# Optimization experiments

Measured on AMD Instinct MI355X. Metric: run time of the kernel, lower is better.

Reference implementation:

```python
import jax, jax.numpy as jnp
import numpy as np

D = 512      # model dim
NH = 8       # heads
DH = 64      # dim per head
M = 256      # num landmarks
ITERS = 6    # pinv iterations
EPS = 1e-5   # layernorm eps


def layer_norm(x, g, b):
    mu = x.mean(-1, keepdims=True)
    var = ((x - mu) ** 2).mean(-1, keepdims=True)
    return (x - mu) * jax.lax.rsqrt(var + EPS) * g + b


def moore_penrose_pinv(x, iters=ITERS):
    abs_x = jnp.abs(x)
    col = abs_x.sum(-1)
    row = abs_x.sum(-2)
    z = jnp.swapaxes(x, -1, -2) / (jnp.max(col) * jnp.max(row))
    I = jnp.eye(x.shape[-1], dtype=x.dtype)
    for _ in range(iters):
        xz = x @ z
        z = 0.25 * z @ (13 * I - xz @ (15 * I - xz @ (7 * I - xz)))
    return z


def nystrom_attention(x, w_qkv, w_out, b_out, res_w):
    B, n0, _ = x.shape
    pad = (M - n0 % M) % M
    x = jnp.pad(x, ((0, 0), (pad, 0), (0, 0)))  # pad at front, like lucidrains
    n = n0 + pad
    qkv = x @ w_qkv  # (B, n, 3*D), no bias
    q, k, v = jnp.split(qkv, 3, axis=-1)
    rs = lambda t: t.reshape(B, n, NH, DH).transpose(0, 2, 1, 3)  # (B,H,n,d)
    q = rs(q) * (DH ** -0.5)
    k = rs(k)
    v = rs(v)
    l = n // M
    q_l = q.reshape(B, NH, M, l, DH).mean(3)  # (B,H,M,d) landmark means
    k_l = k.reshape(B, NH, M, l, DH).mean(3)
    s1 = jnp.einsum('bhnd,bhmd->bhnm', q, k_l)
    s2 = jnp.einsum('bhmd,bhld->bhml', q_l, k_l)
    s3 = jnp.einsum('bhmd,bhnd->bhmn', q_l, k)
    a1 = jax.nn.softmax(s1, -1)
    a2 = jax.nn.softmax(s2, -1)
    a3 = jax.nn.softmax(s3, -1)
    out = a1 @ (moore_penrose_pinv(a2) @ (a3 @ v))  # (B,H,n,d)
    # depthwise residual conv over sequence: Conv2d(heads, heads, (33,1), groups=heads)
    res = jax.lax.conv_general_dilated(v, res_w, (1, 1), 'SAME',
                                       feature_group_count=NH,
                                       dimension_numbers=('NCHW', 'OIHW', 'NCHW'))
    out = out + res
    out = out.transpose(0, 2, 1, 3).reshape(B, n, NH * DH) @ w_out + b_out
    return out[:, -n0:]


def dwconv(x, w, b):
    y = jax.lax.conv_general_dilated(x, w, (1, 1), 'SAME',
                                     feature_group_count=x.shape[1],
                                     dimension_numbers=('NCHW', 'OIHW', 'NCHW'))
    return y + b[None, :, None, None]


def ppeg(x, pw7, pb7, pw5, pb5, pw3, pb3, Hh, Ww):
    cls, feat = x[:, :1], x[:, 1:]
    B, _, C = x.shape
    cnn = feat.transpose(0, 2, 1).reshape(B, C, Hh, Ww)
    y = cnn + dwconv(cnn, pw7, pb7) + dwconv(cnn, pw5, pb5) + dwconv(cnn, pw3, pb3)
    y = y.reshape(B, C, Hh * Ww).transpose(0, 2, 1)
    return jnp.concatenate([cls, y], axis=1)


def _forward(x, w_fc1, b_fc1, cls_token, ln1_g, ln1_b, qkv1_w, out1_w, out1_b, res1_w,
             ln2_g, ln2_b, qkv2_w, out2_w, out2_b, res2_w,
             pw7, pb7, pw5, pb5, pw3, pb3, lnf_g, lnf_b, w_fc2, b_fc2):
    h = jax.nn.relu(x @ w_fc1 + b_fc1)  # (B, N, 512)
    Hn = h.shape[1]
    s = int(np.ceil(np.sqrt(Hn)))  # static grid side
    add = s * s - Hn
    h = jnp.concatenate([h, h[:, :add]], axis=1)
    B = h.shape[0]
    cls = jnp.broadcast_to(cls_token, (B, 1, D))
    h = jnp.concatenate([cls, h], axis=1)
    h = h + nystrom_attention(layer_norm(h, ln1_g, ln1_b), qkv1_w, out1_w, out1_b, res1_w)
    h = ppeg(h, pw7, pb7, pw5, pb5, pw3, pb3, s, s)
    h = h + nystrom_attention(layer_norm(h, ln2_g, ln2_b), qkv2_w, out2_w, out2_b, res2_w)
    h = layer_norm(h, lnf_g, lnf_b)[:, 0]
    return h @ w_fc2 + b_fc2


def setup_inputs() -> dict:
    key = jax.random.key(0)
    ks = jax.random.split(key, 16)
    g = lambda k, shp, s=0.02: jax.random.normal(k, shp, dtype=jnp.float32) * s
    z = lambda n: jnp.zeros((n,), jnp.float32)
    o = lambda n: jnp.ones((n,), jnp.float32)
    B, N, DIN, NC = 2, 10000, 1024, 2
    return {
        'x': jax.random.normal(ks[0], (B, N, DIN), dtype=jnp.float32),
        'w_fc1': g(ks[1], (DIN, D)), 'b_fc1': z(D),
        'cls_token': g(ks[2], (1, 1, D), 1.0),
        'ln1_g': o(D), 'ln1_b': z(D),
        'qkv1_w': g(ks[3], (D, 3 * D)),
        'out1_w': g(ks[4], (D, D)), 'out1_b': z(D),
        'res1_w': g(ks[5], (NH, 1, 33, 1)),
        'ln2_g': o(D), 'ln2_b': z(D),
        'qkv2_w': g(ks[6], (D, 3 * D)),
        'out2_w': g(ks[7], (D, D)), 'out2_b': z(D),
        'res2_w': g(ks[8], (NH, 1, 33, 1)),
        'pw7': g(ks[9], (D, 1, 7, 7)), 'pb7': z(D),
        'pw5': g(ks[10], (D, 1, 5, 5)), 'pb5': z(D),
        'pw3': g(ks[11], (D, 1, 3, 3)), 'pb3': z(D),
        'lnf_g': o(D), 'lnf_b': z(D),
        'w_fc2': g(ks[12], (D, NC)), 'b_fc2': z(NC),
    }


def reference(x, w_fc1, b_fc1, cls_token, ln1_g, ln1_b, qkv1_w, out1_w, out1_b, res1_w,
              ln2_g, ln2_b, qkv2_w, out2_w, out2_b, res2_w,
              pw7, pb7, pw5, pb5, pw3, pb3, lnf_g, lnf_b, w_fc2, b_fc2):
    logits = _forward(x, w_fc1, b_fc1, cls_token, ln1_g, ln1_b, qkv1_w, out1_w, out1_b, res1_w,
                      ln2_g, ln2_b, qkv2_w, out2_w, out2_b, res2_w,
                      pw7, pb7, pw5, pb5, pw3, pb3, lnf_g, lnf_b, w_fc2, b_fc2)
    Y_prob = jax.nn.softmax(logits, -1)
    Y_hat = jnp.argmax(logits, -1)
    return logits, Y_prob, Y_hat
```

## Files before the change

kernel.cpp:

```cpp
#include <hip/hip_runtime.h>
#include <math.h>

#define FLAG_RELU 1
#define FLAG_BIAS 2
#define FLAG_ACC  4
#define FLAG_ATOMIC 8

static constexpr int BB   = 2;
static constexpr int N0   = 10000;
static constexpr int DIN  = 1024;
static constexpr int D    = 512;
static constexpr int NH   = 8;
static constexpr int DH   = 64;
static constexpr int MM   = 256;
static constexpr int SEQ  = 10240;
static constexpr int PADR = 239;
static constexpr int NTOK = 10001;
static constexpr int LL   = 40;
static constexpr float EPS_ = 1e-5f;

typedef short short8v __attribute__((ext_vector_type(8)));
typedef float f32x4 __attribute__((ext_vector_type(4)));

__device__ __forceinline__ void atomicMaxPosF(float* addr, float v) {
    atomicMax((unsigned int*)addr, __float_as_uint(v));
}
__device__ __forceinline__ ushort f2bf(float f) {
    unsigned u = __float_as_uint(f);
    return (ushort)((u + 0x7FFFu + ((u >> 16) & 1u)) >> 16);
}
__device__ __forceinline__ float bf2f(ushort h) {
    return __uint_as_float(((unsigned)h) << 16);
}
__device__ __forceinline__ void split4(float4 f, ushort* ph, ushort* pl) {
    ushort4 hv, lv;
    hv.x = f2bf(f.x); lv.x = f2bf(f.x - bf2f(hv.x));
    hv.y = f2bf(f.y); lv.y = f2bf(f.y - bf2f(hv.y));
    hv.z = f2bf(f.z); lv.z = f2bf(f.z - bf2f(hv.z));
    hv.w = f2bf(f.w); lv.w = f2bf(f.w - bf2f(hv.w));
    *(ushort4*)ph = hv; *(ushort4*)pl = lv;
}

__global__ __launch_bounds__(256)
void mgemm128(const float* __restrict__ A, int lda, long long sAz,
              const ushort* __restrict__ BtH, const ushort* __restrict__ BtL, int ldbt,
              float* __restrict__ C, int ldc, long long sCz, const float* __restrict__ bias,
              int M, int N, int K, int flags, int qcols, float qscale)
{
    __shared__ ushort AsH[4*128*8], AsL[4*128*8], BsH[4*128*8], BsL[4*128*8];
    A += (size_t)blockIdx.z * sAz;
    C += (size_t)blockIdx.z * sCz;
    int t = threadIdx.x;
    int m0 = blockIdx.y * 128, n0 = blockIdx.x * 128;
    int w = t >> 6, lane = t & 63, q = lane >> 4, r = lane & 15;
    int wm = w >> 1, wn = w & 1;
    f32x4 acc[4][4];
    #pragma unroll
    for (int i = 0; i < 4; i++)
        #pragma unroll
        for (int j = 0; j < 4; j++) acc[i][j] = (f32x4){0.f,0.f,0.f,0.f};

    int srow = t >> 1, scg = (t & 1) * 16;
    int qg = (t & 1) * 2;
    int gm = m0 + srow;
    float4 pa0, pa1, pa2, pa3;
    uint4  pb0, pb1, pb2, pb3;
    {
        pa0 = pa1 = pa2 = pa3 = make_float4(0,0,0,0);
        if (gm < M) {
            const float* ap = A + (size_t)gm * lda + scg;
            pa0 = *(const float4*)(ap);   pa1 = *(const float4*)(ap+4);
            pa2 = *(const float4*)(ap+8); pa3 = *(const float4*)(ap+12);
        }
        size_t gb = (size_t)(n0 + srow) * ldbt + scg;
        pb0 = *(const uint4*)(BtH + gb); pb1 = *(const uint4*)(BtH + gb + 8);
        pb2 = *(const uint4*)(BtL + gb); pb3 = *(const uint4*)(BtL + gb + 8);
    }
    for (int k0 = 0; k0 < K; k0 += 32) {
        {
            ushort hb[16], lb[16];
            split4(pa0, &hb[0],  &lb[0]);
            split4(pa1, &hb[4],  &lb[4]);
            split4(pa2, &hb[8],  &lb[8]);
            split4(pa3, &hb[12], &lb[12]);
            *(uint4*)&AsH[(qg  )*1024 + srow*8] = *(uint4*)&hb[0];
            *(uint4*)&AsH[(qg+1)*1024 + srow*8] = *(uint4*)&hb[8];
            *(uint4*)&AsL[(qg  )*1024 + srow*8] = *(uint4*)&lb[0];
            *(uint4*)&AsL[(qg+1)*1024 + srow*8] = *(uint4*)&lb[8];
            *(uint4*)&BsH[(qg  )*1024 + srow*8] = pb0;
            *(uint4*)&BsH[(qg+1)*1024 + srow*8] = pb1;
            *(uint4*)&BsL[(qg  )*1024 + srow*8] = pb2;
            *(uint4*)&BsL[(qg+1)*1024 + srow*8] = pb3;
        }
        __syncthreads();
        if (k0 + 32 < K) {
            pa0 = pa1 = pa2 = pa3 = make_float4(0,0,0,0);
            if (gm < M) {
                const float* ap = A + (size_t)gm * lda + k0 + 32 + scg;
                pa0 = *(const float4*)(ap);   pa1 = *(const float4*)(ap+4);
                pa2 = *(const float4*)(ap+8); pa3 = *(const float4*)(ap+12);
            }
            size_t gb = (size_t)(n0 + srow) * ldbt + k0 + 32 + scg;
            pb0 = *(const uint4*)(BtH + gb); pb1 = *(const uint4*)(BtH + gb + 8);
            pb2 = *(const uint4*)(BtL + gb); pb3 = *(const uint4*)(BtL + gb + 8);
        }
        short8v ah[4], al[4];
        #pragma unroll
        for (int mi = 0; mi < 4; mi++) {
            int row = wm*64 + mi*16 + r;
            ah[mi] = *(const short8v*)&AsH[q*1024 + row*8];
            al[mi] = *(const short8v*)&AsL[q*1024 + row*8];
        }
        #pragma unroll
        for (int ni = 0; ni < 4; ni++) {
            int col = wn*64 + ni*16 + r;
            short8v bh = *(const short8v*)&BsH[q*1024 + col*8];
            short8v bl = *(const short8v*)&BsL[q*1024 + col*8];
            #pragma unroll
            for (int mi = 0; mi < 4; mi++) {
                acc[mi][ni] = __builtin_amdgcn_mfma_f32_16x16x32_bf16(ah[mi], bh, acc[mi][ni], 0,0,0);
                acc[mi][ni] = __builtin_amdgcn_mfma_f32_16x16x32_bf16(ah[mi], bl, acc[mi][ni], 0,0,0);
                acc[mi][ni] = __builtin_amdgcn_mfma_f32_16x16x32_bf16(al[mi], bh, acc[mi][ni], 0,0,0);
            }
        }
        __syncthreads();
    }
    #pragma unroll
    for (int mi = 0; mi < 4; mi++)
        #pragma unroll
        for (int ni = 0; ni < 4; ni++) {
            int gcol = n0 + wn*64 + ni*16 + r;
            float qs = (gcol < qcols) ? qscale : 1.f;
            float bv = (flags & FLAG_BIAS) ? bias[gcol] : 0.f;
            #pragma unroll
            for (int rg = 0; rg < 4; rg++) {
                int grow = m0 + wm*64 + mi*16 + q*4 + rg;
                if (grow >= M) continue;
                float v = acc[mi][ni][rg] * qs + bv;
                if (flags & FLAG_RELU) v = fmaxf(v, 0.f);
                float* cp = C + (size_t)grow * ldc + gcol;
                if (flags & FLAG_ACC) v += *cp;
                *cp = v;
            }
        }
}

__global__ __launch_bounds__(256)
void mbgemm64(const float* __restrict__ Abase, long long sAb, long long sAh, long long sAz, int lda,
              const ushort* __restrict__ BtH, const ushort* __restrict__ BtL,
              const float* __restrict__ Bnt, long long sBb, long long sBh, int ldb,
              float* __restrict__ Cbase, long long sCb, long long sCh, long long sCz, int ldc,
              ushort* __restrict__ eTH, ushort* __restrict__ eTL, long long sT, int ldct,
              int M, int N, int K, int nchunk,
              float dg, float bsc, float osc, int slab0, int flags)
{
    __shared__ ushort AsH[4*64*8], AsL[4*64*8], BsH[4*64*8], BsL[4*64*8];
    int zi = blockIdx.z / nchunk, ch = blockIdx.z % nchunk;
    int g = slab0 + zi, b = g >> 3, h = g & 7;
    const float* A = Abase + (size_t)b*sAb + (size_t)h*sAh + (size_t)zi*sAz;
    float* C = Cbase ? (Cbase + (size_t)b*sCb + (size_t)h*sCh + (size_t)zi*sCz) : nullptr;
    int kpc = K / nchunk;
    int kb = ch * kpc, ke = kb + kpc;
    int t = threadIdx.x;
    int m0 = blockIdx.y * 64, n0 = blockIdx.x * 64;
    int w = t >> 6, lane = t & 63, q = lane >> 4, r = lane & 15;
    int wm = w >> 1, wn = w & 1;
    f32x4 acc[2][2];
    #pragma unroll
    for (int i = 0; i < 2; i++)
        #pragma unroll
        for (int j = 0; j < 2; j++) acc[i][j] = (f32x4){0.f,0.f,0.f,0.f};

    int srow = t >> 2, scg = (t & 3) * 8;
    int qg = t & 3;
    const float* Abp = Bnt ? (Bnt + (size_t)b*sBb + (size_t)h*sBh) : nullptr;
    float4 pa0, pa1;
    float4 pf0, pf1;
    uint4  pu0, pu1;
    {
        const float* ap = A + (size_t)(m0 + srow) * lda + kb + scg;
        pa0 = *(const float4*)ap; pa1 = *(const float4*)(ap+4);
        if (Bnt) {
            const float* bp = Abp + (size_t)(n0 + srow) * ldb + kb + scg;
            pf0 = *(const float4*)bp; pf1 = *(const float4*)(bp+4);
        } else {
            size_t gb = (size_t)b*sBb + (size_t)h*sBh + (size_t)(n0 + srow) * ldb + kb + scg;
            pu0 = *(const uint4*)(BtH + gb); pu1 = *(const uint4*)(BtL + gb);
        }
    }
    for (int k0 = kb; k0 < ke; k0 += 32) {
        {
            ushort hb[8], lb[8];
            split4(pa0, &hb[0], &lb[0]);
            split4(pa1, &hb[4], &lb[4]);
            *(uint4*)&AsH[qg*512 + srow*8] = *(uint4*)&hb[0];
            *(uint4*)&AsL[qg*512 + srow*8] = *(uint4*)&lb[0];
            if (Bnt) {
                ushort hc[8], lc[8];
                split4(pf0, &hc[0], &lc[0]);
                split4(pf1, &hc[4], &lc[4]);
                *(uint4*)&BsH[qg*512 + srow*8] = *(uint4*)&hc[0];
                *(uint4*)&BsL[qg*512 + srow*8] = *(uint4*)&lc[0];
            } else {
                *(uint4*)&BsH[qg*512 + srow*8] = pu0;
                *(uint4*)&BsL[qg*512 + srow*8] = pu1;
            }
        }
        __syncthreads();
        if (k0 + 32 < ke) {
            const float* ap = A + (size_t)(m0 + srow) * lda + k0 + 32 + scg;
            pa0 = *(const float4*)ap; pa1 = *(const float4*)(ap+4);
            if (Bnt) {
                const float* bp = Abp + (size_t)(n0 + srow) * ldb + k0 + 32 + scg;
                pf0 = *(const float4*)bp; pf1 = *(const float4*)(bp+4);
            } else {
                size_t gb = (size_t)b*sBb + (size_t)h*sBh + (size_t)(n0 + srow) * ldb + k0 + 32 + scg;
                pu0 = *(const uint4*)(BtH + gb); pu1 = *(const uint4*)(BtL + gb);
            }
        }
        short8v ah[2], al[2];
        #pragma unroll
        for (int mi = 0; mi < 2; mi++) {
            int row = wm*32 + mi*16 + r;
            ah[mi] = *(const short8v*)&AsH[q*512 + row*8];
            al[mi] = *(const short8v*)&AsL[q*512 + row*8];
        }
        #pragma unroll
        for (int ni = 0; ni < 2; ni++) {
            int col = wn*32 + ni*16 + r;
            short8v bh = *(const short8v*)&BsH[q*512 + col*8];
            short8v bl = *(const short8v*)&BsL[q*512 + col*8];
            #pragma unroll
            for (int mi = 0; mi < 2; mi++) {
                acc[mi][ni] = __builtin_amdgcn_mfma_f32_16x16x32_bf16(ah[mi], bh, acc[mi][ni], 0,0,0);
                acc[mi][ni] = __builtin_amdgcn_mfma_f32_16x16x32_bf16(ah[mi], bl, acc[mi][ni], 0,0,0);
                acc[mi][ni] = __builtin_amdgcn_mfma_f32_16x16x32_bf16(al[mi], bh, acc[mi][ni], 0,0,0);
            }
        }
        __syncthreads();
    }
    bool dgnz = (dg != 0.f);
    #pragma unroll
    for (int mi = 0; mi < 2; mi++)
        #pragma unroll
        for (int ni = 0; ni < 2; ni++) {
            int gm0 = m0 + wm*32 + mi*16 + q*4;
            int gn  = n0 + wn*32 + ni*16 + r;
            float v[4];
            #pragma unroll
            for (int rg = 0; rg < 4; rg++) {
                float u = bsc * acc[mi][ni][rg];
                if (dgnz) u += dg * A[(size_t)(gm0+rg) * lda + gn];
                v[rg] = osc * u;
            }
            if (C) {
                if (flags & FLAG_ATOMIC) {
                    #pragma unroll
                    for (int rg = 0; rg < 4; rg++)
                        atomicAdd(C + (size_t)(gm0+rg) * ldc + gn, v[rg]);
                } else {
                    #pragma unroll
                    for (int rg = 0; rg < 4; rg++)
                        C[(size_t)(gm0+rg) * ldc + gn] = v[rg];
                }
            }
            if (eTH) {
                ushort4 hv, lv;
                hv.x = f2bf(v[0]); lv.x = f2bf(v[0] - bf2f(hv.x));
                hv.y = f2bf(v[1]); lv.y = f2bf(v[1] - bf2f(hv.y));
                hv.z = f2bf(v[2]); lv.z = f2bf(v[2] - bf2f(hv.z));
                hv.w = f2bf(v[3]); lv.w = f2bf(v[3] - bf2f(hv.w));
                size_t to = (size_t)g * sT + (size_t)gn * ldct + gm0;
                *(ushort4*)(eTH + to) = hv;
                *(ushort4*)(eTL + to) = lv;
            }
        }
}

__global__ __launch_bounds__(256)
void convsplitT(const float* __restrict__ in, ushort* __restrict__ oh, ushort* __restrict__ ol,
                int R, int C, int ldin, long long sInB, long long sInH, long long sInZ,
                int ldo, long long sOutZ)
{
    __shared__ float tile[32][33];
    int z = blockIdx.z, b = z >> 3, h = z & 7;
    const float* I = in + (size_t)b*sInB + (size_t)h*sInH + (size_t)z*sInZ;
    int p0 = blockIdx.x * 32, c0 = blockIdx.y * 32;
    int tx = threadIdx.x & 31, ty = threadIdx.x >> 5;
    #pragma unroll
    for (int k = 0; k < 4; k++) {
        int rr = p0 + ty + k*8, cc = c0 + tx;
        tile[ty + k*8][tx] = (rr < R && cc < C) ? I[(size_t)rr * ldin + cc] : 0.f;
    }
    __syncthreads();
    #pragma unroll
    for (int k = 0; k < 4; k++) {
        int rr = p0 + tx, cc = c0 + ty + k*8;
        if (rr < R && cc < C) {
            float f = tile[tx][ty + k*8];
            ushort hv = f2bf(f);
            size_t o = (size_t)z * sOutZ + (size_t)cc * ldo + rr;
            oh[o] = hv; ol[o] = f2bf(f - bf2f(hv));
        }
    }
}

__global__ void fill_cls(const float* __restrict__ cls, float* __restrict__ H) {
    H[(size_t)blockIdx.x * NTOK * D + threadIdx.x] = cls[threadIdx.x];
}

__global__ __launch_bounds__(256)
void ln_pad(const float* __restrict__ H, const float* __restrict__ g,
            const float* __restrict__ bt, float* __restrict__ out)
{
    int blk = blockIdx.x;
    int b = blk / SEQ, i = blk % SEQ;
    int t = threadIdx.x;
    float* orow = out + (size_t)blk * D;
    if (i < PADR) { orow[t] = 0.f; orow[t+256] = 0.f; return; }
    const float* x = H + ((size_t)b * NTOK + (i - PADR)) * D;
    float v0 = x[t], v1 = x[t+256];
    __shared__ float w1[4], w2[4];
    float s = v0 + v1;
    for (int o = 32; o > 0; o >>= 1) s += __shfl_xor(s, o);
    if ((t & 63) == 0) w1[t >> 6] = s;
    __syncthreads();
    float mu = (w1[0]+w1[1]+w1[2]+w1[3]) * (1.0f / D);
    float d0 = v0 - mu, d1 = v1 - mu;
    float qq = d0*d0 + d1*d1;
    for (int o = 32; o > 0; o >>= 1) qq += __shfl_xor(qq, o);
    if ((t & 63) == 0) w2[t >> 6] = qq;
    __syncthreads();
    float rs = rsqrtf((w2[0]+w2[1]+w2[2]+w2[3]) * (1.0f / D) + EPS_);
    orow[t]     = d0 * rs * g[t]     + bt[t];
    orow[t+256] = d1 * rs * g[t+256] + bt[t+256];
}

__global__ __launch_bounds__(512)
void landmarks(const float* __restrict__ qkv, float* __restrict__ ql,
               float* __restrict__ klt, ushort* __restrict__ klH, ushort* __restrict__ klL)
{
    int blk = blockIdx.x;
    int b = blk >> 8, m = blk & 255;
    int c = threadIdx.x;
    const float* base = qkv + ((size_t)b * SEQ + (size_t)m * LL) * 1536;
    float sq0=0,sq1=0,sq2=0,sq3=0, sk0=0,sk1=0,sk2=0,sk3=0;
    for (int tt = 0; tt < LL; tt += 4) {
        const float* rr = base + (size_t)tt * 1536;
        sq0 += rr[c];          sk0 += rr[512 + c];
        sq1 += rr[1536 + c];   sk1 += rr[1536 + 512 + c];
        sq2 += rr[3072 + c];   sk2 += rr[3072 + 512 + c];
        sq3 += rr[4608 + c];   sk3 += rr[4608 + 512 + c];
    }
    float sq = (sq0+sq1+sq2+sq3) * (1.0f / LL);
    float sk = (sk0+sk1+sk2+sk3) * (1.0f / LL);
    int h = c >> 6, d = c & 63;
    int slab = b * NH + h;
    ql [((size_t)slab * MM + m) * DH + d] = sq;
    klt[((size_t)slab * DH + d) * MM + m] = sk;
    size_t kidx = ((size_t)slab * MM + m) * DH + d;
    ushort kh = f2bf(sk);
    klH[kidx] = kh; klL[kidx] = f2bf(sk - bf2f(kh));
}

__global__ __launch_bounds__(256)
void s2_softmax(const float* __restrict__ ql, const float* __restrict__ klt,
                float* __restrict__ a2)
{
    int blk = blockIdx.x;
    int m = blk & 255, slab = blk >> 8;
    int j = threadIdx.x;
    __shared__ float q[64];
    __shared__ float red[256];
    if (j < 64) q[j] = ql[((size_t)slab * MM + m) * DH + j];
    __syncthreads();
    const float* kt = klt + (size_t)slab * DH * MM;
    float s = 0.f;
    #pragma unroll 8
    for (int kk = 0; kk < 64; kk++) s = fmaf(q[kk], kt[kk*MM + j], s);
    red[j] = s; __syncthreads();
    for (int o = 128; o > 0; o >>= 1) { if (j < o) red[j] = fmaxf(red[j], red[j+o]); __syncthreads(); }
    float mx = red[0]; __syncthreads();
    float e = expf(s - mx);
    red[j] = e; __syncthreads();
    for (int o = 128; o > 0; o >>= 1) { if (j < o) red[j] += red[j+o]; __syncthreads(); }
    a2[((size_t)slab * MM + m) * MM + j] = e / red[0];
}

__global__ void zero_scr(float* s) { if (threadIdx.x < 2) s[threadIdx.x] = 0.f; }

__global__ __launch_bounds__(256)
void a2_alpha(const float* __restrict__ a2, float* __restrict__ scr)
{
    int slab = blockIdx.x, t = threadIdx.x;
    const float* A = a2 + (size_t)slab * MM * MM;
    float cs = 0.f, rs = 0.f;
    for (int rr = 0; rr < MM; rr++) cs += fabsf(A[(size_t)rr * MM + t]);
    for (int cc = 0; cc < MM; cc++) rs += fabsf(A[(size_t)t * MM + cc]);
    __shared__ float red[256];
    red[t] = rs; __syncthreads();
    for (int o = 128; o > 0; o >>= 1) { if (t < o) red[t] = fmaxf(red[t], red[t+o]); __syncthreads(); }
    float mrs = red[0]; __syncthreads();
    red[t] = cs; __syncthreads();
    for (int o = 128; o > 0; o >>= 1) { if (t < o) red[t] = fmaxf(red[t], red[t+o]); __syncthreads(); }
    float mcs = red[0];
    if (t == 0) { atomicMaxPosF(scr + 0, mrs); atomicMaxPosF(scr + 1, mcs); }
}

__global__ __launch_bounds__(256)
void z_init(const float* __restrict__ a2, const float* __restrict__ scr,
            float* __restrict__ z, ushort* __restrict__ zTh, ushort* __restrict__ zTl)
{
    size_t idx = (size_t)blockIdx.x * 256 + threadIdx.x;
    int slab = (int)(idx >> 16), rr = (int)((idx >> 8) & 255), cc = (int)(idx & 255);
    float inv = 1.0f / (scr[0] * scr[1]);
    z[idx] = a2[((size_t)slab << 16) + (size_t)cc * MM + rr] * inv;
    float tv = a2[idx] * inv;
    ushort th = f2bf(tv);
    zTh[idx] = th; zTl[idx] = f2bf(tv - bf2f(th));
}

__global__ __launch_bounds__(256)
void s3_softmax(float* __restrict__ s3)
{
    float* row = s3 + (size_t)blockIdx.x * SEQ;
    int t = threadIdx.x;
    float4 v[10];
    #pragma unroll
    for (int i = 0; i < 10; i++) v[i] = *(const float4*)(row + 4*(i*256 + t));
    float mx = -3.4e38f;
    #pragma unroll
    for (int i = 0; i < 10; i++)
        mx = fmaxf(mx, fmaxf(fmaxf(v[i].x, v[i].y), fmaxf(v[i].z, v[i].w)));
    __shared__ float red[4];
    for (int o = 32; o > 0; o >>= 1) mx = fmaxf(mx, __shfl_xor(mx, o));
    if ((t & 63) == 0) red[t >> 6] = mx;
    __syncthreads();
    mx = fmaxf(fmaxf(red[0], red[1]), fmaxf(red[2], red[3]));
    float sum = 0.f;
    #pragma unroll
    for (int i = 0; i < 10; i++) {
        v[i].x = expf(v[i].x - mx); v[i].y = expf(v[i].y - mx);
        v[i].z = expf(v[i].z - mx); v[i].w = expf(v[i].w - mx);
        sum += v[i].x + v[i].y + v[i].z + v[i].w;
    }
    __shared__ float red2[4];
    for (int o = 32; o > 0; o >>= 1) sum += __shfl_xor(sum, o);
    if ((t & 63) == 0) red2[t >> 6] = sum;
    __syncthreads();
    float inv = 1.0f / (red2[0] + red2[1] + red2[2] + red2[3]);
    #pragma unroll
    for (int i = 0; i < 10; i++) {
        v[i].x *= inv; v[i].y *= inv; v[i].z *= inv; v[i].w *= inv;
        *(float4*)(row + 4*(i*256 + t)) = v[i];
    }
}

__global__ __launch_bounds__(256)
void softmax256(float* __restrict__ P)
{
    int wid = threadIdx.x >> 6, lane = threadIdx.x & 63;
    float* p = P + ((size_t)blockIdx.x * 4 + wid) * MM + lane * 4;
    float4 v = *(float4*)p;
    float m = fmaxf(fmaxf(v.x, v.y), fmaxf(v.z, v.w));
    for (int o = 32; o > 0; o >>= 1) m = fmaxf(m, __shfl_xor(m, o));
    v.x = expf(v.x - m); v.y = expf(v.y - m);
    v.z = expf(v.z - m); v.w = expf(v.w - m);
    float s = v.x + v.y + v.z + v.w;
    for (int o = 32; o > 0; o >>= 1) s += __shfl_xor(s, o);
    float inv = 1.0f / s;
    v.x *= inv; v.y *= inv; v.z *= inv; v.w *= inv;
    *(float4*)p = v;
}

__global__ __launch_bounds__(512)
void res_add(const float* __restrict__ qkv, const float* __restrict__ rw,
             float* __restrict__ attn)
{
    int blk = blockIdx.x;
    int b = blk / (SEQ/16), i0 = (blk % (SEQ/16)) * 16;
    int c = threadIdx.x, h = c >> 6;
    __shared__ float w[NH*33];
    if (c < NH*33) w[c] = rw[c];
    __syncthreads();
    float acc[16];
    float* ab = attn + ((size_t)b * SEQ + i0) * D + c;
    #pragma unroll
    for (int rr = 0; rr < 16; rr++) acc[rr] = ab[(size_t)rr * D];
    const float* vb = qkv + (size_t)b * SEQ * 1536 + 2*D + c;
    const float* wh = w + h * 33;
    #pragma unroll 4
    for (int jj = 0; jj < 48; jj++) {
        int j = i0 + jj - 16;
        float val = ((unsigned)j < (unsigned)SEQ) ? vb[(size_t)j * 1536] : 0.f;
        #pragma unroll
        for (int rr = 0; rr < 16; rr++) {
            int ky = jj - rr;
            if (ky >= 0 && ky < 33) acc[rr] = fmaf(val, wh[ky], acc[rr]);
        }
    }
    #pragma unroll
    for (int rr = 0; rr < 16; rr++) ab[(size_t)rr * D] = acc[rr];
}

__global__ __launch_bounds__(256)
void t_fw(const float* __restrict__ H, float* __restrict__ P)
{
    __shared__ float tile[32][33];
    int p0 = blockIdx.x * 32, c0 = blockIdx.y * 32, b = blockIdx.z;
    int tx = threadIdx.x & 31, ty = threadIdx.x >> 5;
    #pragma unroll
    for (int k = 0; k < 4; k++) {
        int pos = p0 + ty + k*8;
        tile[ty + k*8][tx] = (pos < 10000)
            ? H[((size_t)b * NTOK + 1 + pos) * D + c0 + tx] : 0.f;
    }
    __syncthreads();
    #pragma unroll
    for (int k = 0; k < 4; k++) {
        int c = c0 + ty + k*8, pos = p0 + tx;
        if (pos < 10000)
            P[((size_t)b * D + c) * 10000 + pos] = tile[tx][ty + k*8];
    }
}

__global__ __launch_bounds__(256)
void ppeg_conv(const float* __restrict__ P,
               const float* __restrict__ w7, const float* __restrict__ b7,
               const float* __restrict__ w5, const float* __restrict__ b5,
               const float* __restrict__ w3, const float* __restrict__ b3,
               float* __restrict__ Q)
{
    __shared__ float PS[106 * 107];
    __shared__ float w7s[49], w5s[25], w3s[9];
    int blk = blockIdx.x;
    int b = blk >> 9, c = blk & 511;
    int t = threadIdx.x;
    for (int idx = t; idx < 106*107; idx += 256) PS[idx] = 0.f;
    if (t < 49) w7s[t] = w7[(size_t)c * 49 + t];
    if (t < 25) w5s[t] = w5[(size_t)c * 25 + t];
    if (t < 9)  w3s[t] = w3[(size_t)c * 9 + t];
    float bsum = b7[c] + b5[c] + b3[c];
    __syncthreads();
    const float* Pin = P + ((size_t)b * D + c) * 10000;
    for (int p = t; p < 10000; p += 256) {
        int y = p / 100, x = p - y * 100;
        PS[(y + 3) * 107 + x + 3] = Pin[p];
    }
    __syncthreads();
    float* Qo = Q + ((size_t)b * D + c) * 10000;
    for (int task = t; task < 2500; task += 256) {
        int ry = task / 100, x = task - ry * 100;
        int y0 = ry * 4;
        float a0 = bsum + PS[(y0+3)*107 + x+3];
        float a1 = bsum + PS[(y0+4)*107 + x+3];
        float a2 = bsum + PS[(y0+5)*107 + x+3];
        float a3 = bsum + PS[(y0+6)*107 + x+3];
        #pragma unroll
        for (int rr = 0; rr < 10; rr++) {
            const float* rp = &PS[(y0 + rr) * 107 + x];
            #pragma unroll
            for (int kx = 0; kx < 7; kx++) {
                float v = rp[kx];
                if (rr < 7)            a0 = fmaf(v, w7s[rr*7 + kx], a0);
                if (rr >= 1 && rr < 8) a1 = fmaf(v, w7s[(rr-1)*7 + kx], a1);
                if (rr >= 2 && rr < 9) a2 = fmaf(v, w7s[(rr-2)*7 + kx], a2);
                if (rr >= 3)           a3 = fmaf(v, w7s[(rr-3)*7 + kx], a3);
            }
        }
        #pragma unroll
        for (int rr = 0; rr < 8; rr++) {
            const float* rp = &PS[(y0 + rr + 1) * 107 + x + 1];
            #pragma unroll
            for (int kx = 0; kx < 5; kx++) {
                float v = rp[kx];
                if (rr < 5)            a0 = fmaf(v, w5s[rr*5 + kx], a0);
                if (rr >= 1 && rr < 6) a1 = fmaf(v, w5s[(rr-1)*5 + kx], a1);
                if (rr >= 2 && rr < 7) a2 = fmaf(v, w5s[(rr-2)*5 + kx], a2);
                if (rr >= 3)           a3 = fmaf(v, w5s[(rr-3)*5 + kx], a3);
            }
        }
        #pragma unroll
        for (int rr = 0; rr < 6; rr++) {
            const float* rp = &PS[(y0 + rr + 2) * 107 + x + 2];
            #pragma unroll
            for (int kx = 0; kx < 3; kx++) {
                float v = rp[kx];
                if (rr < 3)            a0 = fmaf(v, w3s[rr*3 + kx], a0);
                if (rr >= 1 && rr < 4) a1 = fmaf(v, w3s[(rr-1)*3 + kx], a1);
                if (rr >= 2 && rr < 5) a2 = fmaf(v, w3s[(rr-2)*3 + kx], a2);
                if (rr >= 3)           a3 = fmaf(v, w3s[(rr-3)*3 + kx], a3);
            }
        }
        Qo[(y0+0)*100 + x] = a0;
        Qo[(y0+1)*100 + x] = a1;
        Qo[(y0+2)*100 + x] = a2;
        Qo[(y0+3)*100 + x] = a3;
    }
}

__global__ __launch_bounds__(256)
void t_bw(const float* __restrict__ Q, float* __restrict__ H)
{
    __shared__ float tile[32][33];
    int p0 = blockIdx.x * 32, c0 = blockIdx.y * 32, b = blockIdx.z;
    int tx = threadIdx.x & 31, ty = threadIdx.x >> 5;
    #pragma unroll
    for (int k = 0; k < 4; k++) {
        int c = c0 + ty + k*8, pos = p0 + tx;
        tile[ty + k*8][tx] = (pos < 10000)
            ? Q[((size_t)b * D + c) * 10000 + pos] : 0.f;
    }
    __syncthreads();
    #pragma unroll
    for (int k = 0; k < 4; k++) {
        int pos = p0 + ty + k*8;
        if (pos < 10000)
            H[((size_t)b * NTOK + 1 + pos) * D + c0 + tx] = tile[tx][ty + k*8];
    }
}

__global__ __launch_bounds__(512)
void final_head(const float* __restrict__ H, const float* __restrict__ g,
                const float* __restrict__ bt, const float* __restrict__ w2,
                const float* __restrict__ b2, float* __restrict__ out)
{
    int b = blockIdx.x, t = threadIdx.x;
    __shared__ float red[512];
    float v = H[(size_t)b * NTOK * D + t];
    red[t] = v; __syncthreads();
    for (int o = 256; o > 0; o >>= 1) { if (t < o) red[t] += red[t+o]; __syncthreads(); }
    float mu = red[0] * (1.0f / D); __syncthreads();
    float dv = v - mu;
    red[t] = dv*dv; __syncthreads();
    for (int o = 256; o > 0; o >>= 1) { if (t < o) red[t] += red[t+o]; __syncthreads(); }
    float rstd = rsqrtf(red[0] * (1.0f / D) + EPS_); __syncthreads();
    float xn = dv * rstd * g[t] + bt[t];
    red[t] = xn * w2[2*t]; __syncthreads();
    for (int o = 256; o > 0; o >>= 1) { if (t < o) red[t] += red[t+o]; __syncthreads(); }
    float l0 = red[0] + b2[0]; __syncthreads();
    red[t] = xn * w2[2*t+1]; __syncthreads();
    for (int o = 256; o > 0; o >>= 1) { if (t < o) red[t] += red[t+o]; __syncthreads(); }
    float l1 = red[0] + b2[1];
    if (t == 0) {
        out[b*2+0] = l0; out[b*2+1] = l1;
        float mx = fmaxf(l0, l1);
        float e0 = expf(l0 - mx), e1 = expf(l1 - mx);
        float ssum = e0 + e1;
        out[4 + b*2 + 0] = e0 / ssum;
        out[4 + b*2 + 1] = e1 / ssum;
        out[8 + b] = (l1 > l0) ? 1.0f : 0.0f;
    }
}

extern "C" void kernel_launch(void* const* d_in, const int* in_sizes, int n_in,
                              void* d_out, int out_size, void* d_ws, size_t ws_size,
                              hipStream_t stream)
{
    const float* x      = (const float*)d_in[0];
    const float* w_fc1  = (const float*)d_in[1];
    const float* b_fc1  = (const float*)d_in[2];
    const float* cls    = (const float*)d_in[3];
    const float* ln1_g  = (const float*)d_in[4];
    const float* ln1_b  = (const float*)d_in[5];
    const float* qkv1_w = (const float*)d_in[6];
    const float* out1_w = (const float*)d_in[7];
    const float* out1_b = (const float*)d_in[8];
    const float* res1_w = (const float*)d_in[9];
    const float* ln2_g  = (const float*)d_in[10];
    const float* ln2_b  = (const float*)d_in[11];
    const float* qkv2_w = (const float*)d_in[12];
    const float* out2_w = (const float*)d_in[13];
    const float* out2_b = (const float*)d_in[14];
    const float* res2_w = (const float*)d_in[15];
    const float* pw7 = (const float*)d_in[16];
    const float* pb7 = (const float*)d_in[17];
    const float* pw5 = (const float*)d_in[18];
    const float* pb5 = (const float*)d_in[19];
    const float* pw3 = (const float*)d_in[20];
    const float* pb3 = (const float*)d_in[21];
    const float* lnf_g = (const float*)d_in[22];
    const float* lnf_b = (const float*)d_in[23];
    const float* w_fc2 = (const float*)d_in[24];
    const float* b_fc2 = (const float*)d_in[25];

    float* ws = (float*)d_ws;
    size_t off = 0;
    auto alloc = [&](size_t n) { float* p = ws + off; off += (n + 63) & ~(size_t)63; return p; };
    float* H    = alloc((size_t)BB * NTOK * D);
    float* LN   = alloc((size_t)BB * SEQ * D);
    float* QKV  = alloc((size_t)BB * SEQ * 3 * D);
    float* QL   = alloc((size_t)BB * NH * MM * DH);
    float* KLT  = alloc((size_t)BB * NH * DH * MM);
    float* A2   = alloc((size_t)BB * NH * MM * MM);
    float* ZA   = alloc((size_t)BB * NH * MM * MM);
    float* ZB   = alloc((size_t)BB * NH * MM * MM);
    float* XZ   = alloc((size_t)BB * NH * MM * MM);
    float* A3V  = alloc((size_t)BB * NH * MM * DH);
    float* WB   = alloc((size_t)BB * NH * MM * DH);
    float* S3   = alloc((size_t)8 * MM * SEQ);
    float* SCR  = alloc(64);
    auto ualloc = [&](size_t n) { ushort* p = (ushort*)(ws + off); off += ((n + 127) / 2) & ~(size_t)63; return p; };
    ushort* WTfcH = ualloc((size_t)512 * 1024);
    ushort* WTfcL = ualloc((size_t)512 * 1024);
    ushort* WTqH  = ualloc((size_t)1536 * 512);
    ushort* WTqL  = ualloc((size_t)1536 * 512);
    ushort* WToH  = ualloc((size_t)512 * 512);
    ushort* WToL  = ualloc((size_t)512 * 512);
    ushort* klBH  = ualloc((size_t)16 * MM * DH);
    ushort* klBL  = ualloc((size_t)16 * MM * DH);
    float*  ATTN = LN;
    ushort* VTH  = (ushort*)LN;
    ushort* VTL  = VTH + (size_t)16 * DH * SEQ;
    ushort* A3VTH = (ushort*)ZB;
    ushort* A3VTL = A3VTH + (size_t)16 * DH * MM;
    ushort* WBTH  = A3VTL + (size_t)16 * DH * MM;
    ushort* WBTL  = WBTH  + (size_t)16 * DH * MM;
    ushort* PT   = (ushort*)S3;
    const size_t PS_ = (size_t)16 * 65536;
    ushort* zTAH = PT;            ushort* zTAL = PT + PS_;
    ushort* zTBH = PT + 2*PS_;    ushort* zTBL = PT + 3*PS_;
    ushort* XZTH = PT + 4*PS_;    ushort* XZTL = PT + 5*PS_;
    ushort* T1TH = PT + 6*PS_;    ushort* T1TL = PT + 7*PS_;
    ushort* T2TH = PT + 8*PS_;    ushort* T2TL = PT + 9*PS_;
    (void)ws_size; (void)in_sizes; (void)n_in; (void)out_size;

    convsplitT<<<dim3(32,16,1), 256, 0, stream>>>(w_fc1, WTfcH, WTfcL, 1024, 512, 512, 0,0,0, 1024, 0);
    mgemm128<<<dim3(4, 79, BB), 256, 0, stream>>>(x, DIN, (long long)N0*DIN,
        WTfcH, WTfcL, 1024, H + D, D, (long long)NTOK*D, b_fc1,
        N0, D, DIN, FLAG_BIAS|FLAG_RELU, 0, 1.f);
    fill_cls<<<BB, D, 0, stream>>>(cls, H);

    auto attention = [&](const float* lg, const float* lb,
                         const float* qw, const float* ow,
                         const float* ob, const float* rw)
    {
        convsplitT<<<dim3(16,48,1), 256, 0, stream>>>(qw, WTqH, WTqL, 512, 1536, 1536, 0,0,0, 512, 0);
        convsplitT<<<dim3(16,16,1), 256, 0, stream>>>(ow, WToH, WToL, 512, 512, 512, 0,0,0, 512, 0);
        ln_pad<<<BB*SEQ, 256, 0, stream>>>(H, lg, lb, LN);
        mgemm128<<<dim3(12, 160, 1), 256, 0, stream>>>(LN, D, 0, WTqH, WTqL, D,
            QKV, 3*D, 0, nullptr, BB*SEQ, 3*D, D, 0, D, 0.125f);
        convsplitT<<<dim3(320, 2, 16), 256, 0, stream>>>(QKV + 2*D, VTH, VTL,
            SEQ, DH, 1536, (long long)SEQ*1536, 64, 0, SEQ, (long long)DH*SEQ);
        landmarks<<<BB*MM, 512, 0, stream>>>(QKV, QL, KLT, klBH, klBL);
        s2_softmax<<<BB*NH*MM, 256, 0, stream>>>(QL, KLT, A2);
        zero_scr<<<1, 64, 0, stream>>>(SCR);
        a2_alpha<<<BB*NH, 256, 0, stream>>>(A2, SCR);
        z_init<<<BB*NH*MM*MM/256, 256, 0, stream>>>(A2, SCR, ZA, zTAH, zTAL);
        float* z = ZA; float* zn = ZB;
        ushort *zTcH = zTAH, *zTcL = zTAL, *zTnH = zTBH, *zTnL = zTBL;
        for (int it = 0; it < 6; it++) {
            dim3 g(4, 4, 16);
            mbgemm64<<<g,256,0,stream>>>(A2, 0,0,65536LL, MM,
                zTcH, zTcL, nullptr, 8LL*65536, 65536LL, MM,
                XZ, 0,0,65536LL, MM, XZTH, XZTL, 65536LL, MM,
                MM, MM, MM, 1, 0.f, 1.f, 1.f, 0, 0);
            mbgemm64<<<g,256,0,stream>>>(XZ, 0,0,65536LL, MM,
                XZTH, XZTL, nullptr, 8LL*65536, 65536LL, MM,
                nullptr, 0,0,0, MM, T1TH, T1TL, 65536LL, MM,
                MM, MM, MM, 1, 7.f, -1.f, 1.f, 0, 0);
            mbgemm64<<<g,256,0,stream>>>(XZ, 0,0,65536LL, MM,
                T1TH, T1TL, nullptr, 8LL*65536, 65536LL, MM,
                nullptr, 0,0,0, MM, T2TH, T2TL, 65536LL, MM,
                MM, MM, MM, 1, 15.f, -1.f, 1.f, 0, 0);
            mbgemm64<<<g,256,0,stream>>>(z, 0,0,65536LL, MM,
                T2TH, T2TL, nullptr, 8LL*65536, 65536LL, MM,
                zn, 0,0,65536LL, MM, zTnH, zTnL, 65536LL, MM,
                MM, MM, MM, 1, 13.f, -1.f, 0.25f, 0, 0);
            float* ts = z; z = zn; zn = ts;
            ushort* uh = zTcH; zTcH = zTnH; zTnH = uh;
            ushort* ul = zTcL; zTcL = zTnL; zTnL = ul;
        }
        for (int grp = 0; grp < 2; grp++) {
            int slab0 = grp * 8;
            mbgemm64<<<dim3(160, 4, 8), 256, 0, stream>>>(QL, 8LL*16384, 16384LL, 0, DH,
                nullptr, nullptr, QKV + D, (long long)SEQ*1536, 64LL, 1536,
                S3, 0,0,(long long)MM*SEQ, SEQ, nullptr, nullptr, 0, 0,
                MM, SEQ, DH, 1, 0.f, 1.f, 1.f, slab0, 0);
            s3_softmax<<<8*MM, 256, 0, stream>>>(S3);
            hipMemsetAsync(A3V + (size_t)slab0 * MM * DH, 0,
                           (size_t)8 * MM * DH * sizeof(float), stream);
            mbgemm64<<<dim3(1, 4, 8*16), 256, 0, stream>>>(S3, 0,0,(long long)MM*SEQ, SEQ,
                VTH, VTL, nullptr, 8LL*DH*SEQ, (long long)DH*SEQ, SEQ,
                A3V, 8LL*16384, 16384LL, 0, DH, nullptr, nullptr, 0, 0,
                MM, DH, SEQ, 16, 0.f, 1.f, 1.f, slab0, FLAG_ATOMIC);
        }
        convsplitT<<<dim3(8, 2, 16), 256, 0, stream>>>(A3V, A3VTH, A3VTL,
            MM, DH, DH, 0, 0, 16384LL, MM, 16384LL);
        mbgemm64<<<dim3(1, 4, 16), 256, 0, stream>>>(z, 0,0,65536LL, MM,
            A3VTH, A3VTL, nullptr, 8LL*16384, 16384LL, MM,
            WB, 8LL*16384, 16384LL, 0, DH, WBTH, WBTL, 16384LL, MM,
            MM, DH, MM, 1, 0.f, 1.f, 1.f, 0, 0);
        for (int grp = 0; grp < 2; grp++) {
            int slab0 = grp * 8;
            mbgemm64<<<dim3(4, 160, 8), 256, 0, stream>>>(QKV, (long long)SEQ*1536, 64LL, 0, 1536,
                klBH, klBL, nullptr, 8LL*16384, 16384LL, DH,
                S3, 0,0,(long long)SEQ*MM, MM, nullptr, nullptr, 0, 0,
                SEQ, MM, DH, 1, 0.f, 1.f, 1.f, slab0, 0);
            softmax256<<<8*SEQ/4, 256, 0, stream>>>(S3);
            mbgemm64<<<dim3(1, 160, 8), 256, 0, stream>>>(S3, 0,0,(long long)SEQ*MM, MM,
                WBTH, WBTL, nullptr, 8LL*16384, 16384LL, MM,
                ATTN, (long long)SEQ*D, 64LL, 0, D, nullptr, nullptr, 0, 0,
                SEQ, DH, MM, 1, 0.f, 1.f, 1.f, slab0, 0);
        }
        res_add<<<BB*SEQ/16, 512, 0, stream>>>(QKV, rw, ATTN);
        mgemm128<<<dim3(4, 79, BB), 256, 0, stream>>>(ATTN + (size_t)PADR*D, D, (long long)SEQ*D,
            WToH, WToL, D, H, D, (long long)NTOK*D, ob,
            NTOK, D, D, FLAG_BIAS|FLAG_ACC, 0, 1.f);
    };

    attention(ln1_g, ln1_b, qkv1_w, out1_w, out1_b, res1_w);

    {
        float* Pp = S3;
        float* Qp = S3 + (size_t)BB * D * 10000;
        dim3 tg((10000 + 31)/32, D/32, BB);
        t_fw<<<tg, 256, 0, stream>>>(H, Pp);
        ppeg_conv<<<BB*D, 256, 0, stream>>>(Pp, pw7, pb7, pw5, pb5, pw3, pb3, Qp);
        t_bw<<<tg, 256, 0, stream>>>(Qp, H);
    }

    attention(ln2_g, ln2_b, qkv2_w, out2_w, out2_b, res2_w);

    final_head<<<BB, 512, 0, stream>>>(H, lnf_g, lnf_b, w_fc2, b_fc2, (float*)d_out);
}
```

Before: 2.390 ms.

## Fuse q·k_landmark scores, softmax, and a1@W product into one kernel

Replaces the two-group sequence of S1 GEMM, row softmax and the GEMM with the pinv-weighted matrix with a single a1_fused kernel. Each block computes a 64-token by 256-landmark score tile with split-bf16 MFMA, does the softmax in registers and shared memory, stages unnormalized probabilities in LDS, and multiplies by WB^T before normalizing. This removes the large S1 round-trips through global memory and several launches. In exchange the kernel uses about 68KB of LDS, which limits occupancy, and re-splits P from LDS using uncoalesced strided reads.

Measured after the change: 2.372 ms. Within noise of the previous version (-0.7%).

```diff
diff --git a/kernel.cpp b/kernel.cpp
--- a/kernel.cpp
+++ b/kernel.cpp
@@ -39,6 +39,12 @@
     hv.z = f2bf(f.z); lv.z = f2bf(f.z - bf2f(hv.z));
     hv.w = f2bf(f.w); lv.w = f2bf(f.w - bf2f(hv.w));
     *(ushort4*)ph = hv; *(ushort4*)pl = lv;
+}
+__device__ __forceinline__ void split8r(const float* p, short8v& h, short8v& l) {
+    ushort hb[8], lb[8];
+    split4(*(const float4*)p,     &hb[0], &lb[0]);
+    split4(*(const float4*)(p+4), &hb[4], &lb[4]);
+    h = *(short8v*)hb; l = *(short8v*)lb;
 }
 
 __global__ __launch_bounds__(256)
@@ -278,6 +284,125 @@
 }
 
 __global__ __launch_bounds__(256)
+void a1_fused(const float* __restrict__ qkv,
+              const ushort* __restrict__ klH, const ushort* __restrict__ klL,
+              const ushort* __restrict__ wbH, const ushort* __restrict__ wbL,
+              float* __restrict__ attn)
+{
+    __shared__ float Pc[256*66];
+    __shared__ float redm[4][64];
+    __shared__ float reds[4][64];
+    int g = blockIdx.y, b = g >> 3, h = g & 7;
+    int tok0 = blockIdx.x * 64;
+    int t = threadIdx.x;
+    int w = t >> 6, lane = t & 63, q = lane >> 4, r = lane & 15;
+
+    f32x4 acc[4][4];
+    #pragma unroll
+    for (int i = 0; i < 4; i++)
+        #pragma unroll
+        for (int j = 0; j < 4; j++) acc[i][j] = (f32x4){0.f,0.f,0.f,0.f};
+    #pragma unroll
+    for (int k0 = 0; k0 < 64; k0 += 32) {
+        short8v ah[4], al[4];
+        #pragma unroll
+        for (int mi = 0; mi < 4; mi++) {
+            const float* ap = qkv + ((size_t)b*SEQ + tok0 + mi*16 + r) * 1536
+                            + h*DH + k0 + q*8;
+            split8r(ap, ah[mi], al[mi]);
+        }
+        #pragma unroll
+        for (int ni = 0; ni < 4; ni++) {
+            size_t kb = ((size_t)g*MM + w*64 + ni*16 + r) * DH + k0 + q*8;
+            short8v bh = *(const short8v*)(klH + kb);
+            short8v bl = *(const short8v*)(klL + kb);
+            #pragma unroll
+            for (int mi = 0; mi < 4; mi++) {
+                acc[mi][ni] = __builtin_amdgcn_mfma_f32_16x16x32_bf16(ah[mi], bh, acc[mi][ni], 0,0,0);
+                acc[mi][ni] = __builtin_amdgcn_mfma_f32_16x16x32_bf16(ah[mi], bl, acc[mi][ni], 0,0,0);
+                acc[mi][ni] = __builtin_amdgcn_mfma_f32_16x16x32_bf16(al[mi], bh, acc[mi][ni], 0,0,0);
+            }
+        }
+    }
+    #pragma unroll
+    for (int mi = 0; mi < 4; mi++)
+        #pragma unroll
+        for (int rg = 0; rg < 4; rg++) {
+            float m = fmaxf(fmaxf(acc[mi][0][rg], acc[mi][1][rg]),
+                            fmaxf(acc[mi][2][rg], acc[mi][3][rg]));
+            for (int o = 8; o > 0; o >>= 1) m = fmaxf(m, __shfl_xor(m, o));
+            if (r == 0) redm[w][mi*16 + q*4 + rg] = m;
+        }
+    __syncthreads();
+    #pragma unroll
+    for (int mi = 0; mi < 4; mi++)
+        #pragma unroll
+        for (int rg = 0; rg < 4; rg++) {
+            int row = mi*16 + q*4 + rg;
+            float gm = fmaxf(fmaxf(redm[0][row], redm[1][row]),
+                             fmaxf(redm[2][row], redm[3][row]));
+            float s = 0.f;
+            #pragma unroll
+            for (int ni = 0; ni < 4; ni++) {
+                float e = expf(acc[mi][ni][rg] - gm);
+                acc[mi][ni][rg] = e;
+                s += e;
+            }
+            for (int o = 8; o > 0; o >>= 1) s += __shfl_xor(s, o);
+            if (r == 0) reds[w][row] = s;
+        }
+    #pragma unroll
+    for (int mi = 0; mi < 4; mi++)
+        #pragma unroll
+        for (int ni = 0; ni < 4; ni++) {
+            int col = w*64 + ni*16 + r;
+            int row0 = mi*16 + q*4;
+            float* pp = &Pc[col*66 + row0];
+            *(float2*)(pp)     = make_float2(acc[mi][ni][0], acc[mi][ni][1]);
+            *(float2*)(pp + 2) = make_float2(acc[mi][ni][2], acc[mi][ni][3]);
+        }
+    __syncthreads();
+    f32x4 oacc[4];
+    #pragma unroll
+    for (int ni = 0; ni < 4; ni++) oacc[ni] = (f32x4){0.f,0.f,0.f,0.f};
+    for (int k0 = 0; k0 < 8; k0++) {
+        short8v ph, pl;
+        {
+            ushort hb[8], lb[8];
+            #pragma unroll
+            for (int j = 0; j < 8; j++) {
+                int k = k0*32 + q*8 + j;
+                float p = Pc[k*66 + w*16 + r];
+                hb[j] = f2bf(p); lb[j] = f2bf(p - bf2f(hb[j]));
+            }
+            ph = *(short8v*)hb; pl = *(short8v*)lb;
+        }
+        #pragma unroll
+        for (int ni = 0; ni < 4; ni++) {
+            size_t wo = ((size_t)g*64 + ni*16 + r) * MM + k0*32 + q*8;
+            short8v bh = *(const short8v*)(wbH + wo);
+            short8v bl = *(const short8v*)(wbL + wo);
+            oacc[ni] = __builtin_amdgcn_mfma_f32_16x16x32_bf16(ph, bh, oacc[ni], 0,0,0);
+            oacc[ni] = __builtin_amdgcn_mfma_f32_16x16x32_bf16(ph, bl, oacc[ni], 0,0,0);
+            oacc[ni] = __builtin_amdgcn_mfma_f32_16x16x32_bf16(pl, bh, oacc[ni], 0,0,0);
+        }
+    }
+    float inv[4];
+    #pragma unroll
+    for (int rg = 0; rg < 4; rg++) {
+        int row = w*16 + q*4 + rg;
+        inv[rg] = 1.0f / (reds[0][row] + reds[1][row] + reds[2][row] + reds[3][row]);
+    }
+    #pragma unroll
+    for (int ni = 0; ni < 4; ni++)
+        #pragma unroll
+        for (int rg = 0; rg < 4; rg++) {
+            int tok = tok0 + w*16 + q*4 + rg;
+            attn[((size_t)b*SEQ + tok) * D + h*DH + ni*16 + r] = oacc[ni][rg] * inv[rg];
+        }
+}
+
+__global__ __launch_bounds__(256)
 void convsplitT(const float* __restrict__ in, ushort* __restrict__ oh, ushort* __restrict__ ol,
                 int R, int C, int ldin, long long sInB, long long sInH, long long sInZ,
                 int ldo, long long sOutZ)
@@ -454,23 +579,6 @@
         v[i].x *= inv; v[i].y *= inv; v[i].z *= inv; v[i].w *= inv;
         *(float4*)(row + 4*(i*256 + t)) = v[i];
     }
-}
-
-__global__ __launch_bounds__(256)
-void softmax256(float* __restrict__ P)
-{
-    int wid = threadIdx.x >> 6, lane = threadIdx.x & 63;
-    float* p = P + ((size_t)blockIdx.x * 4 + wid) * MM + lane * 4;
-    float4 v = *(float4*)p;
-    float m = fmaxf(fmaxf(v.x, v.y), fmaxf(v.z, v.w));
-    for (int o = 32; o > 0; o >>= 1) m = fmaxf(m, __shfl_xor(m, o));
-    v.x = expf(v.x - m); v.y = expf(v.y - m);
-    v.z = expf(v.z - m); v.w = expf(v.w - m);
-    float s = v.x + v.y + v.z + v.w;
-    for (int o = 32; o > 0; o >>= 1) s += __shfl_xor(s, o);
-    float inv = 1.0f / s;
-    v.x *= inv; v.y *= inv; v.z *= inv; v.w *= inv;
-    *(float4*)p = v;
 }
 
 __global__ __launch_bounds__(512)
@@ -791,18 +899,7 @@
             A3VTH, A3VTL, nullptr, 8LL*16384, 16384LL, MM,
             WB, 8LL*16384, 16384LL, 0, DH, WBTH, WBTL, 16384LL, MM,
             MM, DH, MM, 1, 0.f, 1.f, 1.f, 0, 0);
-        for (int grp = 0; grp < 2; grp++) {
-            int slab0 = grp * 8;
-            mbgemm64<<<dim3(4, 160, 8), 256, 0, stream>>>(QKV, (long long)SEQ*1536, 64LL, 0, 1536,
-                klBH, klBL, nullptr, 8LL*16384, 16384LL, DH,
-                S3, 0,0,(long long)SEQ*MM, MM, nullptr, nullptr, 0, 0,
-                SEQ, MM, DH, 1, 0.f, 1.f, 1.f, slab0, 0);
-            softmax256<<<8*SEQ/4, 256, 0, stream>>>(S3);
-            mbgemm64<<<dim3(1, 160, 8), 256, 0, stream>>>(S3, 0,0,(long long)SEQ*MM, MM,
-                WBTH, WBTL, nullptr, 8LL*16384, 16384LL, MM,
-                ATTN, (long long)SEQ*D, 64LL, 0, D, nullptr, nullptr, 0, 0,
-                SEQ, DH, MM, 1, 0.f, 1.f, 1.f, slab0, 0);
-        }
+        a1_fused<<<dim3(SEQ/64, 16), 256, 0, stream>>>(QKV, klBH, klBL, WBTH, WBTL, ATTN);
         res_add<<<BB*SEQ/16, 512, 0, stream>>>(QKV, rw, ATTN);
         mgemm128<<<dim3(4, 79, BB), 256, 0, stream>>>(ATTN + (size_t)PADR*D, D, (long long)SEQ*D,
             WToH, WToL, D, H, D, (long long)NTOK*D, ob,
```
